# Performance work log

Measured on AMD Instinct MI355X. Metric: run time of the kernel, lower is better.

Reference implementation:

```python
import jax, jax.numpy as jnp
import numpy as np

NEG_INF = float("-inf")
WINDOW = 5  # window_size in LocalAttention; half = WINDOW // 2 = 2


def setup_inputs() -> dict:
    key = jax.random.key(0)
    kq, kk, kv = jax.random.split(key, 3)
    B, L, H, E = 4, 2048, 8, 64
    queries = jax.random.normal(kq, (B, L, H, E), dtype=jnp.float32)
    keys = jax.random.normal(kk, (B, L, H, E), dtype=jnp.float32)
    values = jax.random.normal(kv, (B, L, H, E), dtype=jnp.float32)
    return {"queries": queries, "keys": keys, "values": values}


def reference(queries, keys, values):
    # queries/keys/values: [B, L, H, E]; dropout is identity (eval mode).
    B, L, H, E = queries.shape
    scale = 1.0 / jnp.sqrt(jnp.asarray(E, dtype=queries.dtype))
    # Shared scores for both branches: [B, H, L, S]
    scores = jnp.einsum("blhe,bshe->bhls", queries, keys)

    # Global (unmasked) branch
    A_global = jax.nn.softmax(scale * scores, axis=-1)

    # Local branch: torch mask allows j in [max(i-2,0), min(i+2,L)) => i-2 <= j <= i+1
    half = WINDOW // 2
    i = jnp.arange(L)[:, None]
    j = jnp.arange(L)[None, :]
    allowed = (j - i >= -half) & (j - i < half)  # [L, L], asymmetric window
    local_scores = jnp.where(allowed, scores, NEG_INF)
    A_local = jax.nn.softmax(scale * local_scores, axis=-1)

    # Sum of the two attention outputs == (A_global + A_local) @ V
    out = jnp.einsum("bhls,bshd->blhd", A_global + A_local, values)
    return out
```

## Files before the change

kernel.cpp:

```cpp
#include <hip/hip_runtime.h>
#include <hip/hip_bf16.h>
#include <stdint.h>


#define LQ 2048
#define HQ 8
#define EQ 64
#define BQ 4
#define BN 64
#define RS (HQ * EQ)
#define SCALE_LOG2E 0.18033688011112042f
#define NTILE (LQ / BN)
#define TILE_U32 2048
#define IMG_U32 (BQ * HQ * NTILE * TILE_U32)
#define BMQ 128

typedef __attribute__((ext_vector_type(8))) short bf16x8;
typedef __attribute__((ext_vector_type(4))) float f32x4;
typedef __attribute__((ext_vector_type(4))) unsigned int u32x4;
typedef __attribute__((ext_vector_type(2))) unsigned int u32x2;

static __device__ __forceinline__ unsigned int f2bf(float f) {
    union { float f; unsigned int u; } c; c.f = f;
    return (c.u + 0x8000u) >> 16;
}
static __device__ __forceinline__ unsigned int pk2(float lo, float hi) {
    union { float f; unsigned int u; } a, b; a.f = lo; b.f = hi;
    return ((a.u + 0x8000u) >> 16) | ((b.u + 0x8000u) & 0xffff0000u);
}
static __device__ __forceinline__ float fexp2(float x) {
    float r;
    asm volatile("v_exp_f32 %0, %1\n\ts_nop 1" : "=v"(r) : "v"(x));
    return r;
}
static __device__ __forceinline__ void gload16(const uint32_t* g, void* l) {
    __builtin_amdgcn_global_load_lds(
        (const __attribute__((address_space(1))) unsigned int*)g,
        (__attribute__((address_space(3))) unsigned int*)l, 16, 0, 0);
}

__global__ __launch_bounds__(256) void prepack_kernel(
    const float* __restrict__ K, const float* __restrict__ V,
    uint32_t* __restrict__ Kimg, uint32_t* __restrict__ Vimg)
{
    __shared__ unsigned short vt[64 * 72];

    const int tid = threadIdx.x;
    const int jc  = blockIdx.x;
    const int bh  = blockIdx.y;
    const int b   = bh >> 3;
    const int h   = bh & 7;
    const int j0  = jc * BN;
    const float* Kbh = K + (size_t)b * LQ * RS + h * EQ;
    const float* Vbh = V + (size_t)b * LQ * RS + h * EQ;
    uint32_t* Kt = Kimg + (size_t)(bh * NTILE + jc) * TILE_U32;
    uint32_t* Vt = Vimg + (size_t)(bh * NTILE + jc) * TILE_U32;

    #pragma unroll
    for (int it = 0; it < 2; ++it) {
        int t2 = tid + it * 256;
        int jr = t2 >> 3, eo = t2 & 7;
        const float* src = Kbh + (size_t)(j0 + jr) * RS + eo * 8;
        float4 a  = *(const float4*)src;
        float4 bv = *(const float4*)(src + 4);
        u32x4 p;
        p.x = pk2(a.x, a.y);   p.y = pk2(a.z, a.w);
        p.z = pk2(bv.x, bv.y); p.w = pk2(bv.z, bv.w);
        *(u32x4*)&Kt[jr * 32 + ((eo ^ (jr & 7)) << 2)] = p;
    }

    {
        const int jr = tid >> 2;
        const int e0 = (tid & 3) * 16;
        const float* src = Vbh + (size_t)(j0 + jr) * RS + e0;
        #pragma unroll
        for (int q = 0; q < 4; ++q) {
            float4 a = *(const float4*)(src + q * 4);
            const int e = e0 + q * 4;
            vt[(e + 0) * 72 + jr] = (unsigned short)f2bf(a.x);
            vt[(e + 1) * 72 + jr] = (unsigned short)f2bf(a.y);
            vt[(e + 2) * 72 + jr] = (unsigned short)f2bf(a.z);
            vt[(e + 3) * 72 + jr] = (unsigned short)f2bf(a.w);
        }
    }
    __syncthreads();

    #pragma unroll
    for (int it = 0; it < 2; ++it) {
        const int i  = tid + it * 256;
        const int e  = i >> 3, jo = i & 7;
        u32x4 p = *(const u32x4*)&vt[e * 72 + jo * 8];
        *(u32x4*)&Vt[e * 32 + ((jo ^ (e & 7)) << 2)] = p;
    }
}

__global__ __launch_bounds__(256, 2) void hybrid_attn_v9(
    const float* __restrict__ Q, const float* __restrict__ K,
    const float* __restrict__ V, const uint32_t* __restrict__ Kimg,
    const uint32_t* __restrict__ Vimg, float* __restrict__ O)
{
    __shared__ unsigned short KV[8192];
    __shared__ unsigned short Pt[4][2048];
    __shared__ float sloc[BMQ][4];

    const int tid  = threadIdx.x;
    const int wave = tid >> 6;
    const int lane = tid & 63;
    const int c    = lane & 15;
    const int g    = lane >> 4;
    const int id   = blockIdx.x;
    const int bh   = (id & 7) * 4 + ((id >> 3) & 3);
    const int qt   = id >> 5;
    const int b    = bh >> 3;
    const int h    = bh & 7;
    const int i0   = qt * BMQ;
    const int c7   = c & 7;
    const int sw3  = c7 << 1;

    const float* Qbh = Q + (size_t)b * LQ * RS + h * EQ;
    const float* Kbh = K + (size_t)b * LQ * RS + h * EQ;
    const float* Vbh = V + (size_t)b * LQ * RS + h * EQ;
    float*       Obh = O + (size_t)b * LQ * RS + h * EQ;

    bf16x8 qf[2][2];
    #pragma unroll
    for (int t = 0; t < 2; ++t) {
        const int iq = i0 + wave * 32 + t * 16 + c;
        const float* qrow = Qbh + (size_t)iq * RS + g * 8;
        #pragma unroll
        for (int f = 0; f < 2; ++f) {
            float4 a  = *(const float4*)(qrow + f * 32);
            float4 bv = *(const float4*)(qrow + f * 32 + 4);
            union { bf16x8 v; unsigned int u[4]; } fr;
            fr.u[0] = pk2(a.x  * SCALE_LOG2E, a.y  * SCALE_LOG2E);
            fr.u[1] = pk2(a.z  * SCALE_LOG2E, a.w  * SCALE_LOG2E);
            fr.u[2] = pk2(bv.x * SCALE_LOG2E, bv.y * SCALE_LOG2E);
            fr.u[3] = pk2(bv.z * SCALE_LOG2E, bv.w * SCALE_LOG2E);
            qf[t][f] = fr.v;
        }
    }

    const int fo0 = c * 64 + ((g ^ c7) << 3);
    const int fo1 = c * 64 + (((4 | g) ^ c7) << 3);

    unsigned short* pw[4];
    #pragma unroll
    for (int n = 0; n < 4; ++n)
        pw[n] = &Pt[wave][c * 64 + ((((n << 2) | g) ^ sw3) << 2)];
    unsigned short* pr0 = &Pt[wave][c * 64 + (((g << 1) ^ sw3) << 2)];
    unsigned short* pr1 = &Pt[wave][c * 64 + (((8 | (g << 1)) ^ sw3) << 2)];

    const uint32_t* kgb = Kimg + (size_t)bh * (NTILE * TILE_U32) + wave * 512 + lane * 4;
    const uint32_t* vgb = Vimg + (size_t)bh * (NTILE * TILE_U32) + wave * 512 + lane * 4;

    f32x4 oacc[2][4];
    #pragma unroll
    for (int t = 0; t < 2; ++t)
        #pragma unroll
        for (int eg = 0; eg < 4; ++eg) oacc[t][eg] = (f32x4){0.f, 0.f, 0.f, 0.f};
    float lsum[2] = {0.f, 0.f};

    for (int jc = 0; jc < NTILE; ++jc) {
        __syncthreads();
        const uint32_t* kg = kgb + (size_t)jc * TILE_U32;
        const uint32_t* vg = vgb + (size_t)jc * TILE_U32;
        gload16(kg,       &KV[wave * 1024]);
        gload16(kg + 256, &KV[wave * 1024 + 512]);
        gload16(vg,       &KV[4096 + wave * 1024]);
        gload16(vg + 256, &KV[4096 + wave * 1024 + 512]);
        __syncthreads();

        bf16x8 kfr[4][2];
        #pragma unroll
        for (int n = 0; n < 4; ++n) {
            kfr[n][0] = *(const bf16x8*)&KV[n * 1024 + fo0];
            kfr[n][1] = *(const bf16x8*)&KV[n * 1024 + fo1];
        }

        #pragma unroll
        for (int t = 0; t < 2; ++t) {
            f32x4 sf[4];
            #pragma unroll
            for (int n = 0; n < 4; ++n) {
                f32x4 acc = (f32x4){0.f, 0.f, 0.f, 0.f};
                acc = __builtin_amdgcn_mfma_f32_16x16x32_bf16(kfr[n][0], qf[t][0], acc, 0, 0, 0);
                acc = __builtin_amdgcn_mfma_f32_16x16x32_bf16(kfr[n][1], qf[t][1], acc, 0, 0, 0);
                sf[n] = acc;
            }
            float ls = 0.f;
            #pragma unroll
            for (int n = 0; n < 4; ++n) {
                float p0 = fexp2(sf[n][0]);
                float p1 = fexp2(sf[n][1]);
                float p2 = fexp2(sf[n][2]);
                float p3 = fexp2(sf[n][3]);
                ls += (p0 + p1) + (p2 + p3);
                u32x2 pkd;
                pkd.x = pk2(p0, p1);
                pkd.y = pk2(p2, p3);
                *(u32x2*)(pw[n] + t * 1024) = pkd;
            }
            lsum[t] += ls;
        }
        asm volatile("s_waitcnt lgkmcnt(0)" ::: "memory");

        bf16x8 pfr[2][2];
        #pragma unroll
        for (int t = 0; t < 2; ++t) {
            pfr[t][0] = *(const bf16x8*)(pr0 + t * 1024);
            pfr[t][1] = *(const bf16x8*)(pr1 + t * 1024);
        }
        #pragma unroll
        for (int eg = 0; eg < 4; ++eg) {
            bf16x8 v0 = *(const bf16x8*)&KV[4096 + eg * 1024 + fo0];
            bf16x8 v1 = *(const bf16x8*)&KV[4096 + eg * 1024 + fo1];
            #pragma unroll
            for (int t = 0; t < 2; ++t) {
                oacc[t][eg] = __builtin_amdgcn_mfma_f32_16x16x32_bf16(v0, pfr[t][0], oacc[t][eg], 0, 0, 0);
                oacc[t][eg] = __builtin_amdgcn_mfma_f32_16x16x32_bf16(v1, pfr[t][1], oacc[t][eg], 0, 0, 0);
            }
        }
    }

    float linv[2];
    #pragma unroll
    for (int t = 0; t < 2; ++t) {
        float l = lsum[t];
        l += __shfl_xor(l, 16);
        l += __shfl_xor(l, 32);
        linv[t] = 1.0f / l;
    }

    {
        const int br = tid >> 1;
        const int i  = i0 + br;
        const float* qrow = Qbh + (size_t)i * RS;
        #pragma unroll
        for (int halfj = 0; halfj < 2; ++halfj) {
            const int jj = (tid & 1) * 2 + halfj;
            const int j  = i - 2 + jj;
            float s = -INFINITY;
            if (j >= 0 && j < LQ) {
                const float* krow = Kbh + (size_t)j * RS;
                float acc = 0.f;
                #pragma unroll
                for (int e = 0; e < 64; e += 4) {
                    float4 qa = *(const float4*)(qrow + e);
                    float4 ka = *(const float4*)(krow + e);
                    acc = fmaf(qa.x, ka.x, acc); acc = fmaf(qa.y, ka.y, acc);
                    acc = fmaf(qa.z, ka.z, acc); acc = fmaf(qa.w, ka.w, acc);
                }
                s = 0.125f * acc;
            }
            sloc[br][jj] = s;
        }
    }
    __syncthreads();

    #pragma unroll
    for (int t = 0; t < 2; ++t) {
        const int row = wave * 32 + t * 16 + c;
        const int i   = i0 + row;
        float s0 = sloc[row][0], s1 = sloc[row][1], s2 = sloc[row][2], s3 = sloc[row][3];
        float mx = fmaxf(fmaxf(s0, s1), fmaxf(s2, s3));
        float w0 = expf(s0 - mx), w1 = expf(s1 - mx);
        float w2 = expf(s2 - mx), w3 = expf(s3 - mx);
        float inv = 1.0f / (w0 + w1 + w2 + w3);
        w0 *= inv; w1 *= inv; w2 *= inv; w3 *= inv;
        const float li = linv[t];
        float* orow = Obh + (size_t)i * RS;
        #pragma unroll
        for (int eg = 0; eg < 4; ++eg) {
            const int e0 = eg * 16 + g * 4;
            float v0 = oacc[t][eg][0] * li;
            float v1 = oacc[t][eg][1] * li;
            float v2 = oacc[t][eg][2] * li;
            float v3 = oacc[t][eg][3] * li;
            if (w0 > 0.f) {
                float4 vv = *(const float4*)(Vbh + (size_t)(i - 2) * RS + e0);
                v0 = fmaf(w0, vv.x, v0); v1 = fmaf(w0, vv.y, v1);
                v2 = fmaf(w0, vv.z, v2); v3 = fmaf(w0, vv.w, v3);
            }
            if (w1 > 0.f) {
                float4 vv = *(const float4*)(Vbh + (size_t)(i - 1) * RS + e0);
                v0 = fmaf(w1, vv.x, v0); v1 = fmaf(w1, vv.y, v1);
                v2 = fmaf(w1, vv.z, v2); v3 = fmaf(w1, vv.w, v3);
            }
            {
                float4 vv = *(const float4*)(Vbh + (size_t)i * RS + e0);
                v0 = fmaf(w2, vv.x, v0); v1 = fmaf(w2, vv.y, v1);
                v2 = fmaf(w2, vv.z, v2); v3 = fmaf(w2, vv.w, v3);
            }
            if (w3 > 0.f) {
                float4 vv = *(const float4*)(Vbh + (size_t)(i + 1) * RS + e0);
                v0 = fmaf(w3, vv.x, v0); v1 = fmaf(w3, vv.y, v1);
                v2 = fmaf(w3, vv.z, v2); v3 = fmaf(w3, vv.w, v3);
            }
            float4 outv; outv.x = v0; outv.y = v1; outv.z = v2; outv.w = v3;
            *(float4*)(orow + e0) = outv;
        }
    }
}

__global__ __launch_bounds__(256) void hybrid_attn_fb(
    const float* __restrict__ Q, const float* __restrict__ K,
    const float* __restrict__ V, float* __restrict__ O)
{
    __shared__ unsigned short Ks[64 * 64];
    __shared__ unsigned short Vt[64 * 64];
    __shared__ unsigned short Ps[4][16 * 64];
    __shared__ float sloc[64][4];

    const int tid  = threadIdx.x;
    const int wave = tid >> 6;
    const int lane = tid & 63;
    const int c    = lane & 15;
    const int g    = lane >> 4;
    const int qt   = blockIdx.x;
    const int bh   = blockIdx.y;
    const int b    = bh >> 3;
    const int h    = bh & 7;
    const int i0   = qt * 64;

    const float* Qbh = Q + (size_t)b * LQ * RS + h * EQ;
    const float* Kbh = K + (size_t)b * LQ * RS + h * EQ;
    const float* Vbh = V + (size_t)b * LQ * RS + h * EQ;
    float*       Obh = O + (size_t)b * LQ * RS + h * EQ;

    bf16x8 qf[2];
    {
        const int iA = i0 + wave * 16 + c;
        const float* qrow = Qbh + (size_t)iA * RS + g * 8;
        #pragma unroll
        for (int f = 0; f < 2; ++f) {
            float4 a  = *(const float4*)(qrow + f * 32);
            float4 bv = *(const float4*)(qrow + f * 32 + 4);
            union { bf16x8 v; unsigned int u[4]; } fr;
            fr.u[0] = pk2(a.x  * SCALE_LOG2E, a.y  * SCALE_LOG2E);
            fr.u[1] = pk2(a.z  * SCALE_LOG2E, a.w  * SCALE_LOG2E);
            fr.u[2] = pk2(bv.x * SCALE_LOG2E, bv.y * SCALE_LOG2E);
            fr.u[3] = pk2(bv.z * SCALE_LOG2E, bv.w * SCALE_LOG2E);
            qf[f] = fr.v;
        }
    }

    int kfo[4][2], vfo[4][2], pfo[2], pso[4][4];
    #pragma unroll
    for (int n = 0; n < 4; ++n)
        #pragma unroll
        for (int f = 0; f < 2; ++f)
            kfo[n][f] = (n * 16 + c) * 64 + ((((f << 2) | g) ^ (c & 7)) << 3);
    #pragma unroll
    for (int eg = 0; eg < 4; ++eg)
        #pragma unroll
        for (int kh = 0; kh < 2; ++kh)
            vfo[eg][kh] = (eg * 16 + c) * 64 + ((((kh << 2) | g) ^ (c & 7)) << 3);
    #pragma unroll
    for (int kh = 0; kh < 2; ++kh)
        pfo[kh] = c * 64 + ((((kh << 2) | g) ^ (c & 7)) << 3);
    #pragma unroll
    for (int r = 0; r < 4; ++r) {
        const int row = g * 4 + r;
        #pragma unroll
        for (int n = 0; n < 4; ++n) {
            const int col = n * 16 + c;
            pso[r][n] = row * 64 + ((((col >> 3) ^ (row & 7)) << 3) | (col & 7));
        }
    }

    f32x4 oacc[4];
    #pragma unroll
    for (int eg = 0; eg < 4; ++eg) oacc[eg] = (f32x4){0.f, 0.f, 0.f, 0.f};
    float l_r[4] = {0.f, 0.f, 0.f, 0.f};

    for (int j0 = 0; j0 < LQ; j0 += BN) {
        __syncthreads();
        #pragma unroll
        for (int it = 0; it < 2; ++it) {
            int t2 = tid + it * 256;
            int jr = t2 >> 3, eo = t2 & 7;
            const float* src = Kbh + (size_t)(j0 + jr) * RS + eo * 8;
            float4 a  = *(const float4*)src;
            float4 bv = *(const float4*)(src + 4);
            u32x4 p;
            p.x = pk2(a.x, a.y);   p.y = pk2(a.z, a.w);
            p.z = pk2(bv.x, bv.y); p.w = pk2(bv.z, bv.w);
            *(u32x4*)&Ks[jr * 64 + ((eo ^ (jr & 7)) << 3)] = p;
        }
        #pragma unroll
        for (int it = 0; it < 2; ++it) {
            int t2 = tid + it * 256;
            int e = t2 & 63, jo = t2 >> 6;
            const float* src = Vbh + (size_t)(j0 + jo * 8) * RS + e;
            float v0 = src[0 * RS], v1 = src[1 * RS], v2 = src[2 * RS], v3 = src[3 * RS];
            float v4 = src[4 * RS], v5 = src[5 * RS], v6 = src[6 * RS], v7 = src[7 * RS];
            u32x4 p;
            p.x = pk2(v0, v1); p.y = pk2(v2, v3);
            p.z = pk2(v4, v5); p.w = pk2(v6, v7);
            *(u32x4*)&Vt[e * 64 + ((jo ^ (e & 7)) << 3)] = p;
        }
        __syncthreads();

        f32x4 sf[4];
        #pragma unroll
        for (int n = 0; n < 4; ++n) {
            bf16x8 k0 = *(const bf16x8*)&Ks[kfo[n][0]];
            bf16x8 k1 = *(const bf16x8*)&Ks[kfo[n][1]];
            f32x4 acc = (f32x4){0.f, 0.f, 0.f, 0.f};
            acc = __builtin_amdgcn_mfma_f32_16x16x32_bf16(qf[0], k0, acc, 0, 0, 0);
            acc = __builtin_amdgcn_mfma_f32_16x16x32_bf16(qf[1], k1, acc, 0, 0, 0);
            sf[n] = acc;
        }
        #pragma unroll
        for (int r = 0; r < 4; ++r) {
            float p0 = fexp2(sf[0][r]);
            float p1 = fexp2(sf[1][r]);
            float p2 = fexp2(sf[2][r]);
            float p3 = fexp2(sf[3][r]);
            l_r[r] += (p0 + p1) + (p2 + p3);
            Ps[wave][pso[r][0]] = (unsigned short)f2bf(p0);
            Ps[wave][pso[r][1]] = (unsigned short)f2bf(p1);
            Ps[wave][pso[r][2]] = (unsigned short)f2bf(p2);
            Ps[wave][pso[r][3]] = (unsigned short)f2bf(p3);
        }
        asm volatile("s_waitcnt lgkmcnt(0)" ::: "memory");

        bf16x8 pf0 = *(const bf16x8*)&Ps[wave][pfo[0]];
        bf16x8 pf1 = *(const bf16x8*)&Ps[wave][pfo[1]];
        #pragma unroll
        for (int eg = 0; eg < 4; ++eg) {
            bf16x8 v0 = *(const bf16x8*)&Vt[vfo[eg][0]];
            bf16x8 v1 = *(const bf16x8*)&Vt[vfo[eg][1]];
            oacc[eg] = __builtin_amdgcn_mfma_f32_16x16x32_bf16(pf0, v0, oacc[eg], 0, 0, 0);
            oacc[eg] = __builtin_amdgcn_mfma_f32_16x16x32_bf16(pf1, v1, oacc[eg], 0, 0, 0);
        }
    }

    #pragma unroll
    for (int r = 0; r < 4; ++r) {
        float l = l_r[r];
        l += __shfl_xor(l, 1);
        l += __shfl_xor(l, 2);
        l += __shfl_xor(l, 4);
        l += __shfl_xor(l, 8);
        l_r[r] = 1.0f / l;
    }

    {
        const int br = tid >> 2;
        const int jj = tid & 3;
        const int i  = i0 + br;
        const int j  = i - 2 + jj;
        float s = -INFINITY;
        if (j >= 0 && j < LQ) {
            const float* qrow = Qbh + (size_t)i * RS;
            const float* krow = Kbh + (size_t)j * RS;
            float acc = 0.f;
            #pragma unroll
            for (int e = 0; e < 64; e += 4) {
                float4 qa = *(const float4*)(qrow + e);
                float4 ka = *(const float4*)(krow + e);
                acc = fmaf(qa.x, ka.x, acc); acc = fmaf(qa.y, ka.y, acc);
                acc = fmaf(qa.z, ka.z, acc); acc = fmaf(qa.w, ka.w, acc);
            }
            s = 0.125f * acc;
        }
        sloc[br][jj] = s;
    }
    __syncthreads();

    #pragma unroll
    for (int r = 0; r < 4; ++r) {
        const int row = wave * 16 + g * 4 + r;
        const int i   = i0 + row;
        float s0 = sloc[row][0], s1 = sloc[row][1], s2 = sloc[row][2], s3 = sloc[row][3];
        float mx = fmaxf(fmaxf(s0, s1), fmaxf(s2, s3));
        float w0 = expf(s0 - mx), w1 = expf(s1 - mx);
        float w2 = expf(s2 - mx), w3 = expf(s3 - mx);
        float inv = 1.0f / (w0 + w1 + w2 + w3);
        w0 *= inv; w1 *= inv; w2 *= inv; w3 *= inv;
        const float li = l_r[r];
        float* orow = Obh + (size_t)i * RS;
        #pragma unroll
        for (int eg = 0; eg < 4; ++eg) {
            const int e = eg * 16 + c;
            float val = oacc[eg][r] * li;
            if (w0 > 0.f) val += w0 * Vbh[(size_t)(i - 2) * RS + e];
            if (w1 > 0.f) val += w1 * Vbh[(size_t)(i - 1) * RS + e];
            if (w2 > 0.f) val += w2 * Vbh[(size_t)(i    ) * RS + e];
            if (w3 > 0.f) val += w3 * Vbh[(size_t)(i + 1) * RS + e];
            orow[e] = val;
        }
    }
}

extern "C" void kernel_launch(void* const* d_in, const int* in_sizes, int n_in,
                              void* d_out, int out_size, void* d_ws, size_t ws_size,
                              hipStream_t stream) {
    (void)in_sizes; (void)n_in; (void)out_size;
    const float* Q = (const float*)d_in[0];
    const float* K = (const float*)d_in[1];
    const float* V = (const float*)d_in[2];
    float* O = (float*)d_out;
    const size_t need = (size_t)2 * IMG_U32 * 4;
    if (ws_size >= need) {
        uint32_t* Kimg = (uint32_t*)d_ws;
        uint32_t* Vimg = Kimg + IMG_U32;
        hipLaunchKernelGGL(prepack_kernel, dim3(NTILE, BQ * HQ), dim3(256), 0, stream,
                           K, V, Kimg, Vimg);
        hipLaunchKernelGGL(hybrid_attn_v9, dim3((LQ / BMQ) * BQ * HQ), dim3(256), 0, stream,
                           Q, K, V, Kimg, Vimg, O);
    } else {
        hipLaunchKernelGGL(hybrid_attn_fb, dim3(LQ / 64, BQ * HQ), dim3(256), 0, stream,
                           Q, K, V, O);
    }
}
```

Before: 155.6 us.

## Prepack K/V in MFMA fragment order and load fragments directly from global

Result: slower. 159.0 us (+2.2%).

```diff
diff --git a/kernel.cpp b/kernel.cpp
--- a/kernel.cpp
+++ b/kernel.cpp
@@ -33,17 +33,12 @@
     asm volatile("v_exp_f32 %0, %1\n\ts_nop 1" : "=v"(r) : "v"(x));
     return r;
 }
-static __device__ __forceinline__ void gload16(const uint32_t* g, void* l) {
-    __builtin_amdgcn_global_load_lds(
-        (const __attribute__((address_space(1))) unsigned int*)g,
-        (__attribute__((address_space(3))) unsigned int*)l, 16, 0, 0);
-}
 
 __global__ __launch_bounds__(256) void prepack_kernel(
     const float* __restrict__ K, const float* __restrict__ V,
     uint32_t* __restrict__ Kimg, uint32_t* __restrict__ Vimg)
 {
-    __shared__ unsigned short vt[64 * 72];
+    __shared__ unsigned short ts[64 * 72];
 
     const int tid = threadIdx.x;
     const int jc  = blockIdx.x;
@@ -66,8 +61,17 @@
         u32x4 p;
         p.x = pk2(a.x, a.y);   p.y = pk2(a.z, a.w);
         p.z = pk2(bv.x, bv.y); p.w = pk2(bv.z, bv.w);
-        *(u32x4*)&Kt[jr * 32 + ((eo ^ (jr & 7)) << 2)] = p;
-    }
+        *(u32x4*)&ts[jr * 72 + eo * 8] = p;
+    }
+    __syncthreads();
+    #pragma unroll
+    for (int it = 0; it < 2; ++it) {
+        int i = tid + it * 256;
+        int n = i >> 7, f = (i >> 6) & 1, g = (i >> 4) & 3, c = i & 15;
+        u32x4 p = *(const u32x4*)&ts[(n * 16 + c) * 72 + f * 32 + g * 8];
+        *(u32x4*)&Kt[(size_t)i * 4] = p;
+    }
+    __syncthreads();
 
     {
         const int jr = tid >> 2;
@@ -77,29 +81,27 @@
         for (int q = 0; q < 4; ++q) {
             float4 a = *(const float4*)(src + q * 4);
             const int e = e0 + q * 4;
-            vt[(e + 0) * 72 + jr] = (unsigned short)f2bf(a.x);
-            vt[(e + 1) * 72 + jr] = (unsigned short)f2bf(a.y);
-            vt[(e + 2) * 72 + jr] = (unsigned short)f2bf(a.z);
-            vt[(e + 3) * 72 + jr] = (unsigned short)f2bf(a.w);
+            ts[(e + 0) * 72 + jr] = (unsigned short)f2bf(a.x);
+            ts[(e + 1) * 72 + jr] = (unsigned short)f2bf(a.y);
+            ts[(e + 2) * 72 + jr] = (unsigned short)f2bf(a.z);
+            ts[(e + 3) * 72 + jr] = (unsigned short)f2bf(a.w);
         }
     }
     __syncthreads();
-
     #pragma unroll
     for (int it = 0; it < 2; ++it) {
-        const int i  = tid + it * 256;
-        const int e  = i >> 3, jo = i & 7;
-        u32x4 p = *(const u32x4*)&vt[e * 72 + jo * 8];
-        *(u32x4*)&Vt[e * 32 + ((jo ^ (e & 7)) << 2)] = p;
-    }
-}
-
-__global__ __launch_bounds__(256, 2) void hybrid_attn_v9(
+        int i = tid + it * 256;
+        int eg = i >> 7, f = (i >> 6) & 1, g = (i >> 4) & 3, c = i & 15;
+        u32x4 p = *(const u32x4*)&ts[(eg * 16 + c) * 72 + f * 32 + g * 8];
+        *(u32x4*)&Vt[(size_t)i * 4] = p;
+    }
+}
+
+__global__ __launch_bounds__(256) void hybrid_attn_v10(
     const float* __restrict__ Q, const float* __restrict__ K,
     const float* __restrict__ V, const uint32_t* __restrict__ Kimg,
     const uint32_t* __restrict__ Vimg, float* __restrict__ O)
 {
-    __shared__ unsigned short KV[8192];
     __shared__ unsigned short Pt[4][2048];
     __shared__ float sloc[BMQ][4];
 
@@ -140,9 +142,6 @@
         }
     }
 
-    const int fo0 = c * 64 + ((g ^ c7) << 3);
-    const int fo1 = c * 64 + (((4 | g) ^ c7) << 3);
-
     unsigned short* pw[4];
     #pragma unroll
     for (int n = 0; n < 4; ++n)
@@ -150,8 +149,8 @@
     unsigned short* pr0 = &Pt[wave][c * 64 + (((g << 1) ^ sw3) << 2)];
     unsigned short* pr1 = &Pt[wave][c * 64 + (((8 | (g << 1)) ^ sw3) << 2)];
 
-    const uint32_t* kgb = Kimg + (size_t)bh * (NTILE * TILE_U32) + wave * 512 + lane * 4;
-    const uint32_t* vgb = Vimg + (size_t)bh * (NTILE * TILE_U32) + wave * 512 + lane * 4;
+    const uint32_t* kim = Kimg + (size_t)bh * (NTILE * TILE_U32) + lane * 4;
+    const uint32_t* vim = Vimg + (size_t)bh * (NTILE * TILE_U32) + lane * 4;
 
     f32x4 oacc[2][4];
     #pragma unroll
@@ -161,20 +160,19 @@
     float lsum[2] = {0.f, 0.f};
 
     for (int jc = 0; jc < NTILE; ++jc) {
-        __syncthreads();
-        const uint32_t* kg = kgb + (size_t)jc * TILE_U32;
-        const uint32_t* vg = vgb + (size_t)jc * TILE_U32;
-        gload16(kg,       &KV[wave * 1024]);
-        gload16(kg + 256, &KV[wave * 1024 + 512]);
-        gload16(vg,       &KV[4096 + wave * 1024]);
-        gload16(vg + 256, &KV[4096 + wave * 1024 + 512]);
-        __syncthreads();
-
-        bf16x8 kfr[4][2];
+        const uint32_t* kg = kim + (size_t)jc * TILE_U32;
+        const uint32_t* vg = vim + (size_t)jc * TILE_U32;
+
+        bf16x8 kfr[4][2], vfr[4][2];
         #pragma unroll
         for (int n = 0; n < 4; ++n) {
-            kfr[n][0] = *(const bf16x8*)&KV[n * 1024 + fo0];
-            kfr[n][1] = *(const bf16x8*)&KV[n * 1024 + fo1];
+            kfr[n][0] = *(const bf16x8*)(kg + (n * 2 + 0) * 256);
+            kfr[n][1] = *(const bf16x8*)(kg + (n * 2 + 1) * 256);
+        }
+        #pragma unroll
+        for (int eg = 0; eg < 4; ++eg) {
+            vfr[eg][0] = *(const bf16x8*)(vg + (eg * 2 + 0) * 256);
+            vfr[eg][1] = *(const bf16x8*)(vg + (eg * 2 + 1) * 256);
         }
 
         #pragma unroll
@@ -212,12 +210,10 @@
         }
         #pragma unroll
         for (int eg = 0; eg < 4; ++eg) {
-            bf16x8 v0 = *(const bf16x8*)&KV[4096 + eg * 1024 + fo0];
-            bf16x8 v1 = *(const bf16x8*)&KV[4096 + eg * 1024 + fo1];
             #pragma unroll
             for (int t = 0; t < 2; ++t) {
-                oacc[t][eg] = __builtin_amdgcn_mfma_f32_16x16x32_bf16(v0, pfr[t][0], oacc[t][eg], 0, 0, 0);
-                oacc[t][eg] = __builtin_amdgcn_mfma_f32_16x16x32_bf16(v1, pfr[t][1], oacc[t][eg], 0, 0, 0);
+                oacc[t][eg] = __builtin_amdgcn_mfma_f32_16x16x32_bf16(vfr[eg][0], pfr[t][0], oacc[t][eg], 0, 0, 0);
+                oacc[t][eg] = __builtin_amdgcn_mfma_f32_16x16x32_bf16(vfr[eg][1], pfr[t][1], oacc[t][eg], 0, 0, 0);
             }
         }
     }
@@ -508,7 +504,7 @@
         uint32_t* Vimg = Kimg + IMG_U32;
         hipLaunchKernelGGL(prepack_kernel, dim3(NTILE, BQ * HQ), dim3(256), 0, stream,
                            K, V, Kimg, Vimg);
-        hipLaunchKernelGGL(hybrid_attn_v9, dim3((LQ / BMQ) * BQ * HQ), dim3(256), 0, stream,
+        hipLaunchKernelGGL(hybrid_attn_v10, dim3((LQ / BMQ) * BQ * HQ), dim3(256), 0, stream,
                            Q, K, V, Kimg, Vimg, O);
     } else {
         hipLaunchKernelGGL(hybrid_attn_fb, dim3(LQ / 64, BQ * HQ), dim3(256), 0, stream,
```
